# Performance work log

Measured on AMD Instinct MI355X. Metric: run time of the kernel, lower is better.

## Reference

```python
import jax, jax.numpy as jnp
import numpy as np
import math

B, T, HID = 2, 2048, 2048
NH, KVH, HD = 16, 4, 128  # num_heads, kv_heads, head_dim


def rotate_half(x):
    x1, x2 = x[..., : x.shape[-1] // 2], x[..., x.shape[-1] // 2 :]
    return jnp.concatenate([-x2, x1], axis=-1)


def setup_inputs() -> dict:
    key = jax.random.key(0)
    ks = jax.random.split(key, 6)
    hidden_states = jax.random.normal(ks[0], (B, T, HID), dtype=jnp.float32)
    # additive causal mask (0 on/below diag, -inf-ish above)
    causal = jnp.triu(jnp.full((T, T), -1e9, dtype=jnp.float32), k=1)
    attention_mask = causal[None, None, :, :]
    # real RoPE angles
    inv_freq = 1.0 / (10000.0 ** (np.arange(0, HD, 2, dtype=np.float32) / HD))
    t = np.arange(T, dtype=np.float32)
    freqs = np.einsum('t,d->td', t, inv_freq)
    emb = np.concatenate([freqs, freqs], axis=-1)  # (T, HD)
    cos = jnp.asarray(np.cos(emb))[None, None, :, :]
    sin = jnp.asarray(np.sin(emb))[None, None, :, :]
    s = 0.02
    Wq = jax.random.normal(ks[1], (HID, NH * HD), dtype=jnp.float32) * s
    Wk = jax.random.normal(ks[2], (HID, KVH * HD), dtype=jnp.float32) * s
    Wv = jax.random.normal(ks[3], (HID, KVH * HD), dtype=jnp.float32) * s
    Wo = jax.random.normal(ks[4], (HID, HID), dtype=jnp.float32) * s
    return dict(hidden_states=hidden_states, attention_mask=attention_mask,
                cos=cos, sin=sin, Wq=Wq, Wk=Wk, Wv=Wv, Wo=Wo)


def reference(hidden_states, attention_mask, cos, sin, Wq, Wk, Wv, Wo):
    b, t, _ = hidden_states.shape
    # projections; weights stored (in, out) so y = x @ W
    q = (hidden_states @ Wq).reshape(b, t, NH, HD).transpose(0, 2, 1, 3)   # (B,H,T,D)
    k = (hidden_states @ Wk).reshape(b, t, KVH, HD).transpose(0, 2, 1, 3)  # (B,Hkv,T,D)
    v = (hidden_states @ Wv).reshape(b, t, KVH, HD).transpose(0, 2, 1, 3)
    # RoPE
    c, s = cos[:, :, :t, :], sin[:, :, :t, :]
    q = q * c + rotate_half(q) * s
    k = k * c + rotate_half(k) * s
    # GQA: repeat_interleave kv heads
    rf = NH // KVH
    k = jnp.repeat(k, rf, axis=1)
    v = jnp.repeat(v, rf, axis=1)
    scores = jnp.einsum('bhtd,bhsd->bhts', q, k) / math.sqrt(HD)
    scores = scores + attention_mask
    probs = jax.nn.softmax(scores.astype(jnp.float32), axis=-1).astype(q.dtype)
    ctx = jnp.einsum('bhts,bhsd->bhtd', probs, v)
    ctx = ctx.transpose(0, 2, 1, 3).reshape(b, t, HID)
    return ctx @ Wo
```

## Files before the change

kernel.cpp:

```cpp
#include <hip/hip_runtime.h>
#include <hip/hip_bf16.h>
#include <math.h>

typedef __bf16 bf16;
typedef __bf16 bf16x4 __attribute__((ext_vector_type(4)));
typedef __bf16 bf16x8 __attribute__((ext_vector_type(8)));
typedef float f32x4 __attribute__((ext_vector_type(4)));

#define B_   2
#define T_   2048
#define HID_ 2048
#define NH_  16
#define KVH_ 4
#define HD_  128

__device__ __forceinline__ void gload_lds16(const bf16* g, bf16* l) {
    __builtin_amdgcn_global_load_lds(
        (const __attribute__((address_space(1))) unsigned int*)g,
        (__attribute__((address_space(3))) unsigned int*)l, 16, 0, 0);
}

__device__ __forceinline__ bf16x8 cat4(bf16x4 a, bf16x4 b) {
    bf16x8 r;
    #pragma unroll
    for (int i = 0; i < 4; i++) { r[i] = a[i]; r[i + 4] = b[i]; }
    return r;
}

__global__ void cast_to_bf16(const float* __restrict__ in, bf16* __restrict__ out, int n4) {
    int i = blockIdx.x * 256 + threadIdx.x;
    if (i < n4) {
        float4 v = ((const float4*)in)[i];
        bf16x4 o = { (bf16)v.x, (bf16)v.y, (bf16)v.z, (bf16)v.w };
        ((bf16x4*)out)[i] = o;
    }
}

__global__ void transpose_cast(const float* __restrict__ in, bf16* __restrict__ out,
                               int N, int rowOff, int outStride) {
    __shared__ float tile[32][33];
    int k0 = blockIdx.x * 32, n0 = blockIdx.y * 32;
    int tx = threadIdx.x & 31, ty = threadIdx.x >> 5;
    for (int i = ty; i < 32; i += 8)
        tile[i][tx] = in[(size_t)(k0 + i) * N + n0 + tx];
    __syncthreads();
    for (int i = ty; i < 32; i += 8)
        out[(size_t)(rowOff + n0 + i) * outStride + (k0 + tx)] = (bf16)tile[tx][i];
}


__global__ __launch_bounds__(256, 2) void gemm_qkv_rope(
    const bf16* __restrict__ A, const bf16* __restrict__ BT,
    const float* __restrict__ cosb, const float* __restrict__ sinb,
    bf16* __restrict__ q, bf16* __restrict__ k, bf16* __restrict__ vT) {
    __shared__ __align__(16) char smem[128 * 136 * 2];
    bf16* As = (bf16*)smem;
    bf16* Bs = As + 128 * 32;
    bf16* Cs = (bf16*)smem;
    const int K = 2048;
    int bm = blockIdx.x * 128, hid = blockIdx.y, bn = hid * 128;
    int tid = threadIdx.x, lane = tid & 63, w = tid >> 6;
    int wm = (w & 1) * 64, wn = (w >> 1) * 64;
    int lm = lane & 15, quad = lane >> 4;
    int c0 = w * 64 + lane, c1 = 256 + c0;
    int r0 = c0 >> 2, g0 = ((c0 & 3) ^ (r0 & 3)) * 8;
    int r1 = c1 >> 2, g1 = ((c1 & 3) ^ (r1 & 3)) * 8;
    const bf16* a0 = A  + (size_t)(bm + r0) * K + g0;
    const bf16* a1 = A  + (size_t)(bm + r1) * K + g1;
    const bf16* b0 = BT + (size_t)(bn + r0) * K + g0;
    const bf16* b1 = BT + (size_t)(bn + r1) * K + g1;
    bf16* lA0 = As + (size_t)(w * 64) * 8;
    bf16* lA1 = As + (size_t)(256 + w * 64) * 8;
    bf16* lB0 = Bs + (size_t)(w * 64) * 8;
    bf16* lB1 = Bs + (size_t)(256 + w * 64) * 8;
    int sx = ((quad ^ (lm & 3)) << 3);
    f32x4 acc[4][4] = {};
    for (int k0 = 0; k0 < K; k0 += 32) {
        gload_lds16(a0, lA0); gload_lds16(a1, lA1);
        gload_lds16(b0, lB0); gload_lds16(b1, lB1);
        a0 += 32; a1 += 32; b0 += 32; b1 += 32;
        __syncthreads();
        bf16x8 af[4], bfr[4];
        #pragma unroll
        for (int mt = 0; mt < 4; mt++) af[mt]  = *(const bf16x8*)&As[(wm + mt*16 + lm) * 32 + sx];
        #pragma unroll
        for (int nt = 0; nt < 4; nt++) bfr[nt] = *(const bf16x8*)&Bs[(wn + nt*16 + lm) * 32 + sx];
        #pragma unroll
        for (int mt = 0; mt < 4; mt++)
            #pragma unroll
            for (int nt = 0; nt < 4; nt++)
                acc[mt][nt] = __builtin_amdgcn_mfma_f32_16x16x32_bf16(af[mt], bfr[nt], acc[mt][nt], 0, 0, 0);
        __syncthreads();
    }
    #pragma unroll
    for (int mt = 0; mt < 4; mt++)
        #pragma unroll
        for (int r = 0; r < 4; r++) {
            int row = wm + mt*16 + quad*4 + r;
            #pragma unroll
            for (int nt = 0; nt < 4; nt++)
                Cs[row * 136 + wn + nt*16 + lm] = (bf16)acc[mt][nt][r];
        }
    __syncthreads();

    int b = bm >> 11, t0 = bm & 2047;
    if (hid < 20) {
        bool isq = hid < 16;
        int d = (tid & 15) * 8;
        float sgn = (d < 64) ? -1.f : 1.f;
        float scl = isq ? 0.12752965013239224f : 1.0f;
        bf16* dst = isq ? (q + ((size_t)(b * NH_ + hid) * T_) * HD_)
                        : (k + ((size_t)(b * KVH_ + (hid - 16)) * T_) * HD_);
        #pragma unroll
        for (int i = 0; i < 8; i++) {
            int row = (tid >> 4) + i * 16;
            int t = t0 + row;
            bf16x8 x  = *(const bf16x8*)&Cs[row * 136 + d];
            bf16x8 xo = *(const bf16x8*)&Cs[row * 136 + (d ^ 64)];
            bf16x8 o;
            #pragma unroll
            for (int j = 0; j < 8; j++) {
                float c = cosb[t * 128 + d + j], s = sinb[t * 128 + d + j];
                o[j] = (bf16)(((float)x[j] * c + sgn * (float)xo[j] * s) * scl);
            }
            *(bf16x8*)(dst + (size_t)t * HD_ + d) = o;
        }
    } else {
        int kvh = hid - 20;
        int t6 = (tid & 15) * 4;
        int C = 4 * (t6 >> 5) + ((t6 >> 2) & 3);
        int j0 = 4 * ((t6 >> 4) & 1);
        int pos = 8 * C + j0;
        bf16* dst = vT + (size_t)(b * KVH_ + kvh) * HD_ * T_;
        #pragma unroll
        for (int i = 0; i < 8; i++) {
            int d = (tid >> 4) + i * 16;
            #pragma unroll
            for (int half = 0; half < 2; half++) {
                int tt = half * 64 + t6;
                bf16x4 vv = { Cs[(tt+0)*136 + d], Cs[(tt+1)*136 + d],
                              Cs[(tt+2)*136 + d], Cs[(tt+3)*136 + d] };
                *(bf16x4*)(dst + (size_t)d * T_ + t0 + half * 64 + pos) = vv;
            }
        }
    }
}

__global__ __launch_bounds__(256, 2) void gemm_bf16_nt(
    const bf16* __restrict__ A, const bf16* __restrict__ BT, float* __restrict__ C,
    int M, int N, int K) {
    __shared__ __align__(16) bf16 As[128 * 32];
    __shared__ __align__(16) bf16 Bs[128 * 32];
    int bm = blockIdx.x * 128, bn = blockIdx.y * 128;
    int tid = threadIdx.x, lane = tid & 63, w = tid >> 6;
    int wm = (w & 1) * 64, wn = (w >> 1) * 64;
    int lm = lane & 15, quad = lane >> 4;
    int c0 = w * 64 + lane, c1 = 256 + c0;
    int r0 = c0 >> 2, g0 = ((c0 & 3) ^ (r0 & 3)) * 8;
    int r1 = c1 >> 2, g1 = ((c1 & 3) ^ (r1 & 3)) * 8;
    const bf16* a0 = A  + (size_t)(bm + r0) * K + g0;
    const bf16* a1 = A  + (size_t)(bm + r1) * K + g1;
    const bf16* b0 = BT + (size_t)(bn + r0) * K + g0;
    const bf16* b1 = BT + (size_t)(bn + r1) * K + g1;
    bf16* lA0 = As + (size_t)(w * 64) * 8;
    bf16* lA1 = As + (size_t)(256 + w * 64) * 8;
    bf16* lB0 = Bs + (size_t)(w * 64) * 8;
    bf16* lB1 = Bs + (size_t)(256 + w * 64) * 8;
    int sx = ((quad ^ (lm & 3)) << 3);
    f32x4 acc[4][4] = {};
    for (int k0 = 0; k0 < K; k0 += 32) {
        gload_lds16(a0, lA0); gload_lds16(a1, lA1);
        gload_lds16(b0, lB0); gload_lds16(b1, lB1);
        a0 += 32; a1 += 32; b0 += 32; b1 += 32;
        __syncthreads();
        bf16x8 af[4], bfr[4];
        #pragma unroll
        for (int mt = 0; mt < 4; mt++) af[mt]  = *(const bf16x8*)&As[(wm + mt*16 + lm) * 32 + sx];
        #pragma unroll
        for (int nt = 0; nt < 4; nt++) bfr[nt] = *(const bf16x8*)&Bs[(wn + nt*16 + lm) * 32 + sx];
        #pragma unroll
        for (int mt = 0; mt < 4; mt++)
            #pragma unroll
            for (int nt = 0; nt < 4; nt++)
                acc[mt][nt] = __builtin_amdgcn_mfma_f32_16x16x32_bf16(af[mt], bfr[nt], acc[mt][nt], 0, 0, 0);
        __syncthreads();
    }
    #pragma unroll
    for (int mt = 0; mt < 4; mt++) {
        #pragma unroll
        for (int r = 0; r < 4; r++) {
            int row = bm + wm + mt*16 + quad*4 + r;
            float* cp = C + (size_t)row * N + bn + wn + lm;
            #pragma unroll
            for (int nt = 0; nt < 4; nt++)
                cp[nt*16] = acc[mt][nt][r];
        }
    }
}

__global__ __launch_bounds__(256, 2) void flash_attn(
    const bf16* __restrict__ q, const bf16* __restrict__ k, const bf16* __restrict__ vT,
    bf16* __restrict__ ctx) {
    __shared__ __align__(16) bf16 Ks[64 * 128];
    __shared__ __align__(16) bf16 Vp[128 * 64];
    int bh = blockIdx.y;
    int b = bh >> 4, h = bh & 15, kvh = h >> 2;
    int tid = threadIdx.x, lane = tid & 63, w = tid >> 6;
    int lm = lane & 15, quad = lane >> 4, kq = quad * 8;
    const bf16* kg = k  + (size_t)(b * KVH_ + kvh) * T_ * HD_;
    const bf16* vg = vT + (size_t)(b * KVH_ + kvh) * HD_ * T_;
    int ksl = lane >> 4;
    int kko = ((lane >> 2) & 3) * 32;
    int kc  = ((lane & 3) ^ ((lane >> 4) & 3)) * 8;
    int vdl = lane >> 3;
    int vc  = ((lane & 7) ^ ((lane >> 3) & 7)) * 8;
    int sxk = (quad ^ (lm & 3)) << 3;
    int sxv1 = ((quad ^ (lm & 7)) << 3);
    int sxv2 = (((4 + quad) ^ (lm & 7)) << 3);

    for (int half = 0; half < 2; half++) {
        int qt = (half == 0) ? blockIdx.x : (31 - blockIdx.x);
        const bf16* qg = q + ((size_t)(b * NH_ + h) * T_ + qt*64 + w*16 + lm) * HD_;
        bf16x8 qf[4];
        #pragma unroll
        for (int kk = 0; kk < 4; kk++) qf[kk] = *(const bf16x8*)(qg + kk*32 + kq);

        f32x4 Ot[8] = {};
        float l_ = 0.f;
        int nIter = qt + 1;

        for (int it = 0; it < nIter; it++) {
            int s0 = it * 64;
            #pragma unroll
            for (int i = 0; i < 4; i++) {
                int srow = w * 16 + i * 4;
                gload_lds16(kg + (size_t)(s0 + srow + ksl) * HD_ + kko + kc, Ks + srow * 128);
            }
            #pragma unroll
            for (int i = 0; i < 4; i++) {
                int drow = w * 32 + i * 8;
                gload_lds16(vg + (size_t)(drow + vdl) * T_ + s0 + vc, Vp + drow * 64);
            }
            __syncthreads();

            f32x4 sacc[4] = {};
            #pragma unroll
            for (int n = 0; n < 4; n++)
                #pragma unroll
                for (int kk = 0; kk < 4; kk++) {
                    bf16x8 kf = *(const bf16x8*)&Ks[(n*16 + lm) * 128 + kk*32 + sxk];
                    sacc[n] = __builtin_amdgcn_mfma_f32_16x16x32_bf16(kf, qf[kk], sacc[n], 0, 0, 0);
                }
            if (it == qt) {
                #pragma unroll
                for (int n = 0; n < 4; n++)
                    #pragma unroll
                    for (int r = 0; r < 4; r++)
                        if (n*16 + quad*4 + r > w*16 + lm) sacc[n][r] = -1e30f;
            }
            bf16x4 pt[4];
            #pragma unroll
            for (int n = 0; n < 4; n++) {
                f32x4 pe;
                #pragma unroll
                for (int r = 0; r < 4; r++) pe[r] = exp2f(sacc[n][r]);
                l_ += (pe[0] + pe[1]) + (pe[2] + pe[3]);
                #pragma unroll
                for (int r = 0; r < 4; r++) pt[n][r] = (bf16)pe[r];
            }
            bf16x8 pf01 = cat4(pt[0], pt[1]);
            bf16x8 pf23 = cat4(pt[2], pt[3]);
            #pragma unroll
            for (int dt = 0; dt < 8; dt++) {
                const bf16* vr = &Vp[(dt*16 + lm) * 64];
                bf16x8 vf01 = *(const bf16x8*)(vr + sxv1);
                Ot[dt] = __builtin_amdgcn_mfma_f32_16x16x32_bf16(vf01, pf01, Ot[dt], 0, 0, 0);
                bf16x8 vf23 = *(const bf16x8*)(vr + sxv2);
                Ot[dt] = __builtin_amdgcn_mfma_f32_16x16x32_bf16(vf23, pf23, Ot[dt], 0, 0, 0);
            }
            __syncthreads();
        }

        l_ += __shfl_xor(l_, 16);
        l_ += __shfl_xor(l_, 32);
        float linv = 1.0f / l_;
        bf16* cp = ctx + ((size_t)(b * T_) + qt*64 + w*16 + lm) * HID_ + h * HD_;
        #pragma unroll
        for (int dt = 0; dt < 8; dt++) {
            bf16x4 o4 = { (bf16)(Ot[dt][0]*linv), (bf16)(Ot[dt][1]*linv),
                          (bf16)(Ot[dt][2]*linv), (bf16)(Ot[dt][3]*linv) };
            *(bf16x4*)(cp + dt*16 + quad*4) = o4;
        }
    }
}

extern "C" void kernel_launch(void* const* d_in, const int* in_sizes, int n_in,
                              void* d_out, int out_size, void* d_ws, size_t ws_size,
                              hipStream_t stream) {
    const float* hidden = (const float*)d_in[0];
    const float* cosb = (const float*)d_in[2];
    const float* sinb = (const float*)d_in[3];
    const float* Wq = (const float*)d_in[4];
    const float* Wk = (const float*)d_in[5];
    const float* Wv = (const float*)d_in[6];
    const float* Wo = (const float*)d_in[7];
    float* out = (float*)d_out;

    char* ws = (char*)d_ws;
    size_t off = 0;
    bf16* hid_bf = (bf16*)(ws + off); off += (size_t)4096*2048*2;
    bf16* WqkvT  = (bf16*)(ws + off); off += (size_t)3072*2048*2;
    bf16* WoT    = (bf16*)(ws + off); off += (size_t)2048*2048*2;
    bf16* qbuf   = (bf16*)(ws + off); off += (size_t)B_*NH_*T_*HD_*2;
    bf16* kbuf   = (bf16*)(ws + off); off += (size_t)B_*KVH_*T_*HD_*2;
    bf16* vtbuf  = (bf16*)(ws + off); off += (size_t)B_*KVH_*HD_*T_*2;
    bf16* ctx    = (bf16*)(ws + off); off += (size_t)4096*2048*2;

    cast_to_bf16<<<8192, 256, 0, stream>>>(hidden, hid_bf, 4096*2048/4);
    transpose_cast<<<dim3(64, 64), 256, 0, stream>>>(Wq, WqkvT, 2048, 0,    2048);
    transpose_cast<<<dim3(64, 16), 256, 0, stream>>>(Wk, WqkvT, 512,  2048, 2048);
    transpose_cast<<<dim3(64, 16), 256, 0, stream>>>(Wv, WqkvT, 512,  2560, 2048);
    transpose_cast<<<dim3(64, 64), 256, 0, stream>>>(Wo, WoT,   2048, 0,    2048);

    gemm_qkv_rope<<<dim3(32, 24), 256, 0, stream>>>(hid_bf, WqkvT, cosb, sinb, qbuf, kbuf, vtbuf);
    flash_attn<<<dim3(16, 32), 256, 0, stream>>>(qbuf, kbuf, vtbuf, ctx);
    gemm_bf16_nt<<<dim3(32, 16), 256, 0, stream>>>(ctx, WoT, out, 4096, 2048, 2048);
}
```

Measured before the change: 330.0 us.

## Double-buffer K/V tiles in flash attention and retune LDS swizzles

The flash attention loop now uses two LDS buffers for K and V, prefetching the next tile before computing on the current one. This overlaps global loads with MFMA work and drops one barrier per iteration. The K tile swizzle changes to a full 16-way XOR pattern, and the GEMM kernels use a different XOR swizzle based on row pairs, both aimed at reducing LDS bank conflicts. The doubled LDS footprint (64KB for attention) may reduce occupancy.

```diff
diff --git a/kernel.cpp b/kernel.cpp
--- a/kernel.cpp
+++ b/kernel.cpp
@@ -47,6 +47,7 @@
     for (int i = ty; i < 32; i += 8)
         out[(size_t)(rowOff + n0 + i) * outStride + (k0 + tx)] = (bf16)tile[tx][i];
 }
+
 
 
 __global__ __launch_bounds__(256, 2) void gemm_qkv_rope(
@@ -63,8 +64,8 @@
     int wm = (w & 1) * 64, wn = (w >> 1) * 64;
     int lm = lane & 15, quad = lane >> 4;
     int c0 = w * 64 + lane, c1 = 256 + c0;
-    int r0 = c0 >> 2, g0 = ((c0 & 3) ^ (r0 & 3)) * 8;
-    int r1 = c1 >> 2, g1 = ((c1 & 3) ^ (r1 & 3)) * 8;
+    int r0 = c0 >> 2, g0 = (((c0 & 3) ^ ((c0 >> 3) & 3)) * 8);
+    int r1 = c1 >> 2, g1 = (((c1 & 3) ^ ((c1 >> 3) & 3)) * 8);
     const bf16* a0 = A  + (size_t)(bm + r0) * K + g0;
     const bf16* a1 = A  + (size_t)(bm + r1) * K + g1;
     const bf16* b0 = BT + (size_t)(bn + r0) * K + g0;
@@ -73,7 +74,7 @@
     bf16* lA1 = As + (size_t)(256 + w * 64) * 8;
     bf16* lB0 = Bs + (size_t)(w * 64) * 8;
     bf16* lB1 = Bs + (size_t)(256 + w * 64) * 8;
-    int sx = ((quad ^ (lm & 3)) << 3);
+    int sx = ((quad ^ ((lm >> 1) & 3)) << 3);
     f32x4 acc[4][4] = {};
     for (int k0 = 0; k0 < K; k0 += 32) {
         gload_lds16(a0, lA0); gload_lds16(a1, lA1);
@@ -156,8 +157,8 @@
     int wm = (w & 1) * 64, wn = (w >> 1) * 64;
     int lm = lane & 15, quad = lane >> 4;
     int c0 = w * 64 + lane, c1 = 256 + c0;
-    int r0 = c0 >> 2, g0 = ((c0 & 3) ^ (r0 & 3)) * 8;
-    int r1 = c1 >> 2, g1 = ((c1 & 3) ^ (r1 & 3)) * 8;
+    int r0 = c0 >> 2, g0 = (((c0 & 3) ^ ((c0 >> 3) & 3)) * 8);
+    int r1 = c1 >> 2, g1 = (((c1 & 3) ^ ((c1 >> 3) & 3)) * 8);
     const bf16* a0 = A  + (size_t)(bm + r0) * K + g0;
     const bf16* a1 = A  + (size_t)(bm + r1) * K + g1;
     const bf16* b0 = BT + (size_t)(bn + r0) * K + g0;
@@ -166,7 +167,7 @@
     bf16* lA1 = As + (size_t)(256 + w * 64) * 8;
     bf16* lB0 = Bs + (size_t)(w * 64) * 8;
     bf16* lB1 = Bs + (size_t)(256 + w * 64) * 8;
-    int sx = ((quad ^ (lm & 3)) << 3);
+    int sx = ((quad ^ ((lm >> 1) & 3)) << 3);
     f32x4 acc[4][4] = {};
     for (int k0 = 0; k0 < K; k0 += 32) {
         gload_lds16(a0, lA0); gload_lds16(a1, lA1);
@@ -201,8 +202,8 @@
 __global__ __launch_bounds__(256, 2) void flash_attn(
     const bf16* __restrict__ q, const bf16* __restrict__ k, const bf16* __restrict__ vT,
     bf16* __restrict__ ctx) {
-    __shared__ __align__(16) bf16 Ks[64 * 128];
-    __shared__ __align__(16) bf16 Vp[128 * 64];
+    __shared__ __align__(16) bf16 Ksb[2 * 64 * 128];
+    __shared__ __align__(16) bf16 Vpb[2 * 128 * 64];
     int bh = blockIdx.y;
     int b = bh >> 4, h = bh & 15, kvh = h >> 2;
     int tid = threadIdx.x, lane = tid & 63, w = tid >> 6;
@@ -210,13 +211,26 @@
     const bf16* kg = k  + (size_t)(b * KVH_ + kvh) * T_ * HD_;
     const bf16* vg = vT + (size_t)(b * KVH_ + kvh) * HD_ * T_;
     int ksl = lane >> 4;
-    int kko = ((lane >> 2) & 3) * 32;
-    int kc  = ((lane & 3) ^ ((lane >> 4) & 3)) * 8;
     int vdl = lane >> 3;
-    int vc  = ((lane & 7) ^ ((lane >> 3) & 7)) * 8;
-    int sxk = (quad ^ (lm & 3)) << 3;
+    int vc  = (((lane & 7) ^ (vdl & 7)) << 3);
     int sxv1 = ((quad ^ (lm & 7)) << 3);
     int sxv2 = (((4 + quad) ^ (lm & 7)) << 3);
+
+    auto stage = [&](int s0, int p) {
+        bf16* kd = Ksb + p * (64 * 128);
+        bf16* vd = Vpb + p * (128 * 64);
+        #pragma unroll
+        for (int i = 0; i < 4; i++) {
+            int srow = w * 16 + i * 4;
+            int kc = (((lane & 15) ^ (i * 4 + ksl)) << 3);
+            gload_lds16(kg + (size_t)(s0 + srow + ksl) * HD_ + kc, kd + srow * 128);
+        }
+        #pragma unroll
+        for (int i = 0; i < 4; i++) {
+            int drow = w * 32 + i * 8;
+            gload_lds16(vg + (size_t)(drow + vdl) * T_ + s0 + vc, vd + drow * 64);
+        }
+    };
 
     for (int half = 0; half < 2; half++) {
         int qt = (half == 0) ? blockIdx.x : (31 - blockIdx.x);
@@ -229,26 +243,21 @@
         float l_ = 0.f;
         int nIter = qt + 1;
 
+        __syncthreads();
+        stage(0, 0);
+
         for (int it = 0; it < nIter; it++) {
-            int s0 = it * 64;
-            #pragma unroll
-            for (int i = 0; i < 4; i++) {
-                int srow = w * 16 + i * 4;
-                gload_lds16(kg + (size_t)(s0 + srow + ksl) * HD_ + kko + kc, Ks + srow * 128);
-            }
-            #pragma unroll
-            for (int i = 0; i < 4; i++) {
-                int drow = w * 32 + i * 8;
-                gload_lds16(vg + (size_t)(drow + vdl) * T_ + s0 + vc, Vp + drow * 64);
-            }
             __syncthreads();
+            if (it + 1 < nIter) stage((it + 1) * 64, (it + 1) & 1);
+            const bf16* ks = Ksb + (it & 1) * (64 * 128);
+            const bf16* vp = Vpb + (it & 1) * (128 * 64);
 
             f32x4 sacc[4] = {};
             #pragma unroll
             for (int n = 0; n < 4; n++)
                 #pragma unroll
                 for (int kk = 0; kk < 4; kk++) {
-                    bf16x8 kf = *(const bf16x8*)&Ks[(n*16 + lm) * 128 + kk*32 + sxk];
+                    bf16x8 kf = *(const bf16x8*)&ks[(n*16 + lm) * 128 + (((kk*4 + quad) ^ lm) << 3)];
                     sacc[n] = __builtin_amdgcn_mfma_f32_16x16x32_bf16(kf, qf[kk], sacc[n], 0, 0, 0);
                 }
             if (it == qt) {
@@ -272,13 +281,12 @@
             bf16x8 pf23 = cat4(pt[2], pt[3]);
             #pragma unroll
             for (int dt = 0; dt < 8; dt++) {
-                const bf16* vr = &Vp[(dt*16 + lm) * 64];
+                const bf16* vr = &vp[(dt*16 + lm) * 64];
                 bf16x8 vf01 = *(const bf16x8*)(vr + sxv1);
                 Ot[dt] = __builtin_amdgcn_mfma_f32_16x16x32_bf16(vf01, pf01, Ot[dt], 0, 0, 0);
                 bf16x8 vf23 = *(const bf16x8*)(vr + sxv2);
                 Ot[dt] = __builtin_amdgcn_mfma_f32_16x16x32_bf16(vf23, pf23, Ot[dt], 0, 0, 0);
             }
-            __syncthreads();
         }
 
         l_ += __shfl_xor(l_, 16);
```

After: 309.9 us. 1.06x faster.
